# Optimization experiments

Hardware: AMD Instinct MI355X
Metric: run time of the kernel (lower is better)

Reference implementation:

```python
import jax, jax.numpy as jnp
import numpy as np

N = 10000
E = 320000
NDIM_IN = 128
EDIM = 128
NDIM_OUT = 128
HID = 152  # size_embedding
NCLS = 15  # nbclasses


def _lin(k, out_f, in_f, scale=0.05):
    kw, kb = jax.random.split(k)
    W = jax.random.normal(kw, (out_f, in_f), dtype=jnp.float32) * scale
    b = jax.random.normal(kb, (out_f,), dtype=jnp.float32) * scale
    return W, b


def setup_inputs() -> dict:
    key = jax.random.key(0)
    ks = jax.random.split(key, 12)
    nfeats = jax.random.normal(ks[0], (N, 1, NDIM_IN), dtype=jnp.float32)
    efeats = jax.random.normal(ks[1], (E, 1, EDIM), dtype=jnp.float32)
    src = jax.random.randint(ks[2], (E,), 0, N)
    dst = jax.random.randint(ks[3], (E,), 0, N)
    # SAGE layer 1: msg (ndim_in+edim -> 152), apply (ndim_in+152 -> 152)
    Wm1, bm1 = _lin(ks[4], HID, NDIM_IN + EDIM)
    Wa1, ba1 = _lin(ks[5], HID, NDIM_IN + HID)
    # layer 2: msg (152+edim -> 152), apply (152+152 -> 152)
    Wm2, bm2 = _lin(ks[6], HID, HID + EDIM)
    Wa2, ba2 = _lin(ks[7], HID, HID + HID)
    # layer 3: msg (152+edim -> ndim_out), apply (152+ndim_out -> ndim_out)
    Wm3, bm3 = _lin(ks[8], NDIM_OUT, HID + EDIM)
    Wa3, ba3 = _lin(ks[9], NDIM_OUT, HID + NDIM_OUT)
    # edge predictor: Linear(2*ndim_out -> nbclasses)
    Wp, bp = _lin(ks[10], NCLS, 2 * NDIM_OUT)
    return {"nfeats": nfeats, "efeats": efeats, "src": src, "dst": dst,
            "Wm1": Wm1, "bm1": bm1, "Wa1": Wa1, "ba1": ba1,
            "Wm2": Wm2, "bm2": bm2, "Wa2": Wa2, "ba2": ba2,
            "Wm3": Wm3, "bm3": bm3, "Wa3": Wa3, "ba3": ba3,
            "Wp": Wp, "bp": bp}


def _sage_layer(h, e, src, dst, Wm, bm, Wa, ba):
    # h: [N,1,din]  e: [E,1,edim]
    msg = jnp.concatenate([h[src], e], axis=-1) @ Wm.T + bm  # [E,1,dout]
    agg = jax.ops.segment_sum(msg, dst, num_segments=N)       # [N,1,dout]
    deg = jax.ops.segment_sum(jnp.ones((E,), dtype=h.dtype), dst, num_segments=N)
    h_neigh = agg / jnp.maximum(deg, 1.0)[:, None, None]      # mean; 0 for isolated nodes
    return jax.nn.relu(jnp.concatenate([h, h_neigh], axis=-1) @ Wa.T + ba)


def reference(nfeats, efeats, src, dst,
              Wm1, bm1, Wa1, ba1, Wm2, bm2, Wa2, ba2,
              Wm3, bm3, Wa3, ba3, Wp, bp):
    h = _sage_layer(nfeats, efeats, src, dst, Wm1, bm1, Wa1, ba1)
    h = _sage_layer(h, efeats, src, dst, Wm2, bm2, Wa2, ba2)  # dropout is identity in eval
    h = _sage_layer(h, efeats, src, dst, Wm3, bm3, Wa3, ba3)
    h = h.sum(axis=1)  # [N, ndim_out]
    v = jnp.concatenate([h[src], h[dst]], axis=1)  # [E, 2*ndim_out]
    return v @ Wp.T + bp  # [E, nbclasses]
```

## Files before the change

kernel.cpp:

```cpp
#include <hip/hip_runtime.h>
#include <hip/hip_bf16.h>
#include <cstdint>


static inline int cdiv(int a, int b) { return (a + b - 1) / b; }

#define NN 10000
#define NE 320000
#define MTB 313
#define MD 192

typedef __attribute__((ext_vector_type(8))) short bf16x8;
typedef __attribute__((ext_vector_type(4))) float f32x4;

__device__ __forceinline__ ushort f2bf(float x) {
  union { float f; unsigned u; } c; c.f = x;
  unsigned r = c.u + 0x7FFFu + ((c.u >> 16) & 1u);
  return (ushort)(r >> 16);
}
__device__ __forceinline__ float bf2f(unsigned h) {
  union { unsigned u; float f; } c; c.u = h << 16;
  return c.f;
}
__device__ __forceinline__ f32x4 mfma3(bf16x8 ah, bf16x8 al, bf16x8 bh, bf16x8 bl,
                                       f32x4 acc) {
  acc = __builtin_amdgcn_mfma_f32_16x16x32_bf16(ah, bh, acc, 0, 0, 0);
  acc = __builtin_amdgcn_mfma_f32_16x16x32_bf16(al, bh, acc, 0, 0, 0);
  acc = __builtin_amdgcn_mfma_f32_16x16x32_bf16(ah, bl, acc, 0, 0, 0);
  return acc;
}
__device__ __forceinline__ void ld32frag(const float* p, bf16x8& h, bf16x8& l) {
  float4 x0 = *(const float4*)p;
  float4 x1 = *(const float4*)(p + 4);
  float v[8] = {x0.x, x0.y, x0.z, x0.w, x1.x, x1.y, x1.z, x1.w};
#pragma unroll
  for (int j = 0; j < 8; ++j) {
    ushort hh = f2bf(v[j]);
    h[j] = (short)hh;
    l[j] = (short)f2bf(v[j] - bf2f(hh));
  }
}
__device__ __forceinline__ void wpack4(ushort* lds, int base, int KT, int row,
                                       int k0, float4 v) {
  int idx0 = base + ((k0 >> 5) * 4 + ((k0 >> 3) & 3)) * 256 + row * 8 + (k0 & 7);
  int idx1 = idx0 + KT * 1024;
  ushort h0 = f2bf(v.x), h1 = f2bf(v.y), h2 = f2bf(v.z), h3 = f2bf(v.w);
  uint2 uh, ul;
  uh.x = (unsigned)h0 | ((unsigned)h1 << 16);
  uh.y = (unsigned)h2 | ((unsigned)h3 << 16);
  ushort l0 = f2bf(v.x - bf2f(h0)), l1 = f2bf(v.y - bf2f(h1));
  ushort l2 = f2bf(v.z - bf2f(h2)), l3 = f2bf(v.w - bf2f(h3));
  ul.x = (unsigned)l0 | ((unsigned)l1 << 16);
  ul.y = (unsigned)l2 | ((unsigned)l3 << 16);
  *reinterpret_cast<uint2*>(&lds[idx0]) = uh;
  *reinterpret_cast<uint2*>(&lds[idx1]) = ul;
}
__device__ __forceinline__ bf16x8 rfrag(const ushort* lds, int base, int KT,
                                        int plane, int kt, int lane, int mh) {
  int idx = base + ((plane * KT + kt) * 4 + (lane >> 4)) * 256 +
            ((lane & 15) + 16 * mh) * 8;
  return *reinterpret_cast<const bf16x8*>(&lds[idx]);
}

__global__ __launch_bounds__(256) void k_bucket(const int* __restrict__ src,
                                                const int* __restrict__ dst,
                                                int* __restrict__ fill,
                                                int2* __restrict__ bk) {
  int e = blockIdx.x * 256 + threadIdx.x;
  if (e < NE) {
    int d = dst[e];
    int pos = atomicAdd(&fill[d], 1);
    if (pos < MD) bk[d * MD + pos] = make_int2(e, src[e]);
  }
}

struct WDesc {
  const float* W; ushort* hi; ushort* lo;
  int dout, KA, KApad, KB, Korig, NG16, KT, pred;
};
struct PrepArgs {
  WDesc d[7];
  int* fill;
};

__global__ __launch_bounds__(256) void k_prep(PrepArgs P) {
  const int y = blockIdx.y;
  if (y == 7) {
    int i = blockIdx.x * 256 + threadIdx.x;
    if (i < NN) P.fill[i] = 0;
    return;
  }
  const WDesc d = P.d[y];
  int tid = blockIdx.x * 256 + threadIdx.x;
  if (tid >= d.KT * d.NG16 * 64) return;
  int lane = tid & 63;
  int g = (tid >> 6) % d.NG16;
  int t = (tid >> 6) / d.NG16;
  int col = g * 16 + (lane & 15);
  int kbase = t * 32 + ((lane >> 4) * 8);
  size_t o = (size_t)tid * 8;
#pragma unroll
  for (int j = 0; j < 8; ++j) {
    int kk = kbase + j;
    float w = 0.f;
    if (!d.pred) {
      if (col < d.dout) {
        if (kk < d.KApad) { if (kk < d.KA) w = d.W[(size_t)col * d.Korig + kk]; }
        else { int kb = kk - d.KApad; if (kb < d.KB) w = d.W[(size_t)col * d.Korig + d.KA + kb]; }
      }
    } else {
      if (col < 15) w = d.W[(size_t)col * 256 + kk];
      else if (col < 30) w = d.W[(size_t)(col - 15) * 256 + 128 + kk];
    }
    ushort h = f2bf(w);
    d.hi[o + j] = h;
    d.lo[o + j] = f2bf(w - bf2f(h));
  }
}

__global__ __launch_bounds__(1024) void k_eaggpe(
    const float* __restrict__ efeats, const int2* __restrict__ bk,
    const int* __restrict__ fill, const float* __restrict__ nfeats,
    const ushort* __restrict__ Wm1h, const ushort* __restrict__ Wm1l,
    const ushort* __restrict__ pW1h, const ushort* __restrict__ pW1l,
    const ushort* __restrict__ pW2h, const ushort* __restrict__ pW2l,
    const ushort* __restrict__ pW3h, const ushort* __restrict__ pW3l,
    const float* __restrict__ bm1, const float* __restrict__ bm2,
    const float* __restrict__ bm3, float* __restrict__ deg_g,
    ushort* __restrict__ ph1, float* __restrict__ pe1,
    float* __restrict__ pe2, float* __restrict__ pe3) {
  __shared__ ushort efrag[2 * 4 * 1024];
  __shared__ float sdeg[32];
  const int tid = threadIdx.x;
  const int wid = tid >> 6, lane = tid & 63;
  const int row0 = blockIdx.x * 32;
  const int half = lane >> 5, cl = lane & 31;
#pragma unroll
  for (int i = 0; i < 2; ++i) {
    const int r = wid * 2 + i;
    const int d = row0 + r;
    float4 acc[8];
#pragma unroll
    for (int u = 0; u < 8; ++u) acc[u] = make_float4(0.f, 0.f, 0.f, 0.f);
    int cntd = 0;
    if (d < NN) {
      cntd = fill[d];
      const int n = min(cntd, MD);
      const int s = d * MD, t = s + n;
      int j = s;
      for (; j + 15 < t; j += 16) {
#pragma unroll
        for (int u = 0; u < 8; ++u) {
          int e0 = bk[j + 2 * u + half].x;
          float4 v = *(const float4*)(efeats + (size_t)e0 * 128 + cl * 4);
          acc[u].x += v.x; acc[u].y += v.y; acc[u].z += v.z; acc[u].w += v.w;
        }
      }
      for (; j + 1 < t; j += 2) {
        int e0 = bk[j + half].x;
        float4 v = *(const float4*)(efeats + (size_t)e0 * 128 + cl * 4);
        acc[0].x += v.x; acc[0].y += v.y; acc[0].z += v.z; acc[0].w += v.w;
      }
      if (j < t && half == 0) {
        int e0 = bk[j].x;
        float4 v = *(const float4*)(efeats + (size_t)e0 * 128 + cl * 4);
        acc[0].x += v.x; acc[0].y += v.y; acc[0].z += v.z; acc[0].w += v.w;
      }
    }
#pragma unroll
    for (int u = 4; u > 0; u >>= 1)
#pragma unroll
      for (int w = 0; w < u; ++w) {
        acc[w].x += acc[w + u].x; acc[w].y += acc[w + u].y;
        acc[w].z += acc[w + u].z; acc[w].w += acc[w + u].w;
      }
    float4 sm = acc[0];
    sm.x += __shfl_xor(sm.x, 32);
    sm.y += __shfl_xor(sm.y, 32);
    sm.z += __shfl_xor(sm.z, 32);
    sm.w += __shfl_xor(sm.w, 32);
    if (lane < 32) wpack4(efrag, 0, 4, r, cl * 4, sm);
    if (lane == 0) {
      sdeg[r] = (float)cntd;
      if (d < NN) deg_g[d] = (float)cntd;
    }
  }
  __syncthreads();
  const int rA = lane & 15, kl = (lane >> 4) * 8, colL = lane & 15;
  const int r0 = min(row0 + rA, NN - 1), r1 = min(row0 + 16 + rA, NN - 1);
  for (int j = wid; j < 19; j += 16) {
    const ushort *Wh, *Wl;
    const float* bm = nullptr;
    float* pe = nullptr;
    int NG16 = 10, ng0, WPAD = 160, dout = 152;
    bool proj = false;
    if (j < 5) { proj = true; Wh = Wm1h; Wl = Wm1l; ng0 = j * 2; }
    else if (j < 10) { Wh = pW1h; Wl = pW1l; bm = bm1; pe = pe1; ng0 = (j - 5) * 2; }
    else if (j < 15) { Wh = pW2h; Wl = pW2l; bm = bm2; pe = pe2; ng0 = (j - 10) * 2; }
    else { Wh = pW3h; Wl = pW3l; bm = bm3; pe = pe3; ng0 = (j - 15) * 2;
           NG16 = 8; WPAD = 128; dout = 128; }
    f32x4 a00 = {0.f, 0.f, 0.f, 0.f}, a01 = {0.f, 0.f, 0.f, 0.f};
    f32x4 a10 = {0.f, 0.f, 0.f, 0.f}, a11 = {0.f, 0.f, 0.f, 0.f};
#pragma unroll
    for (int kt = 0; kt < 4; ++kt) {
      bf16x8 a0h, a0l, a1h, a1l;
      if (proj) {
        ld32frag(nfeats + (size_t)r0 * 128 + kt * 32 + kl, a0h, a0l);
        ld32frag(nfeats + (size_t)r1 * 128 + kt * 32 + kl, a1h, a1l);
      } else {
        a0h = rfrag(efrag, 0, 4, 0, kt, lane, 0);
        a0l = rfrag(efrag, 0, 4, 1, kt, lane, 0);
        a1h = rfrag(efrag, 0, 4, 0, kt, lane, 1);
        a1l = rfrag(efrag, 0, 4, 1, kt, lane, 1);
      }
      size_t wb = ((size_t)(kt * NG16 + ng0) * 64 + lane) * 8;
      bf16x8 b0h = *(const bf16x8*)(Wh + wb), b0l = *(const bf16x8*)(Wl + wb);
      bf16x8 b1h = *(const bf16x8*)(Wh + wb + 512), b1l = *(const bf16x8*)(Wl + wb + 512);
      a00 = mfma3(a0h, a0l, b0h, b0l, a00);
      a01 = mfma3(a0h, a0l, b1h, b1l, a01);
      a10 = mfma3(a1h, a1l, b0h, b0l, a10);
      a11 = mfma3(a1h, a1l, b1h, b1l, a11);
    }
#pragma unroll
    for (int ms = 0; ms < 2; ++ms) {
      const f32x4 aN0 = ms ? a10 : a00;
      const f32x4 aN1 = ms ? a11 : a01;
#pragma unroll
      for (int reg = 0; reg < 4; ++reg) {
        int rloc = ms * 16 + (lane >> 4) * 4 + reg;
        int row = row0 + rloc;
        if (row >= NN) continue;
#pragma unroll
        for (int ns = 0; ns < 2; ++ns) {
          int col = (ng0 + ns) * 16 + colL;
          float v = ns ? aN1[reg] : aN0[reg];
          if (proj) {
            ph1[(size_t)row * 160 + col] = f2bf(col < 152 ? v : 0.f);
          } else {
            pe[(size_t)row * WPAD + col] =
                (col < dout) ? v + sdeg[rloc] * bm[col] : 0.f;
          }
        }
      }
    }
  }
}

template <int WP>
__global__ __launch_bounds__(64) void k_gath(const ushort* __restrict__ ph,
                                             const float* __restrict__ pe,
                                             const float* __restrict__ deg,
                                             const int2* __restrict__ bk,
                                             const int* __restrict__ fill,
                                             ushort* __restrict__ nmh,
                                             ushort* __restrict__ nml) {
  constexpr int PAIRS = WP / 2;
  constexpr int NV = (PAIRS + 63) / 64;
  const int d = blockIdx.x, lane = threadIdx.x;
  const int n = min(fill[d], MD);
  const int s = d * MD, t = s + n;
  float2 acc[NV][4];
#pragma unroll
  for (int v = 0; v < NV; ++v)
#pragma unroll
    for (int u = 0; u < 4; ++u) acc[v][u] = make_float2(0.f, 0.f);
  int j = s;
  for (; j + 3 < t; j += 4) {
    int s0 = bk[j].y, s1 = bk[j + 1].y, s2 = bk[j + 2].y, s3 = bk[j + 3].y;
#pragma unroll
    for (int v = 0; v < NV; ++v) {
      int p = lane + 64 * v;
      if (p < PAIRS) {
        unsigned x0 = *(const unsigned*)(ph + (size_t)s0 * WP + 2 * p);
        unsigned x1 = *(const unsigned*)(ph + (size_t)s1 * WP + 2 * p);
        unsigned x2 = *(const unsigned*)(ph + (size_t)s2 * WP + 2 * p);
        unsigned x3 = *(const unsigned*)(ph + (size_t)s3 * WP + 2 * p);
        acc[v][0].x += bf2f(x0 & 0xffffu); acc[v][0].y += bf2f(x0 >> 16);
        acc[v][1].x += bf2f(x1 & 0xffffu); acc[v][1].y += bf2f(x1 >> 16);
        acc[v][2].x += bf2f(x2 & 0xffffu); acc[v][2].y += bf2f(x2 >> 16);
        acc[v][3].x += bf2f(x3 & 0xffffu); acc[v][3].y += bf2f(x3 >> 16);
      }
    }
  }
  for (; j < t; ++j) {
    int s0 = bk[j].y;
#pragma unroll
    for (int v = 0; v < NV; ++v) {
      int p = lane + 64 * v;
      if (p < PAIRS) {
        unsigned x0 = *(const unsigned*)(ph + (size_t)s0 * WP + 2 * p);
        acc[v][0].x += bf2f(x0 & 0xffffu); acc[v][0].y += bf2f(x0 >> 16);
      }
    }
  }
  const float inv = 1.f / fmaxf(deg[d], 1.f);
#pragma unroll
  for (int v = 0; v < NV; ++v) {
    int p = lane + 64 * v;
    if (p < PAIRS) {
      float sx = (acc[v][0].x + acc[v][1].x) + (acc[v][2].x + acc[v][3].x);
      float sy = (acc[v][0].y + acc[v][1].y) + (acc[v][2].y + acc[v][3].y);
      float2 pv = *(const float2*)(pe + (size_t)d * WP + 2 * p);
      float nx = (sx + pv.x) * inv, ny = (sy + pv.y) * inv;
      size_t o = (size_t)d * WP + 2 * p;
      ushort hx = f2bf(nx), hy = f2bf(ny);
      *(unsigned*)(nmh + o) = (unsigned)hx | ((unsigned)hy << 16);
      *(unsigned*)(nml + o) =
          (unsigned)f2bf(nx - bf2f(hx)) | ((unsigned)f2bf(ny - bf2f(hy)) << 16);
    }
  }
}

template <int KTH, int KTNM, int NGA, int NGP, bool PRED, bool A32>
__global__ __launch_bounds__(NGA * 32) void k_applyproj(
    const ushort* __restrict__ Ahi, const ushort* __restrict__ Alo,
    const float* __restrict__ Af,
    const ushort* __restrict__ nmh, const ushort* __restrict__ nml,
    const ushort* __restrict__ Wah, const ushort* __restrict__ Wal,
    const float* __restrict__ ba,
    ushort* __restrict__ Yhi, ushort* __restrict__ Ylo,
    const ushort* __restrict__ Wnh, const ushort* __restrict__ Wnl,
    ushort* __restrict__ phout, float* __restrict__ hsd,
    int dout_a, int dout_p) {
  constexpr int KTO = NGA / 2;
  constexpr int OSTR = KTO * 32;
  constexpr int SA = KTH * 32, SB = KTNM * 32;
  constexpr int OSTR2 = NGP * 16;
  __shared__ ushort lds[2 * KTO * 1024];
  const int tid = threadIdx.x;
  const int wid = tid >> 6, lane = tid & 63;
  const int rA = lane & 15, kl = (lane >> 4) * 8, colL = lane & 15;
  const int q = lane >> 4;
  const int row0 = blockIdx.x * 32;
  const int r0 = min(row0 + rA, NN - 1), r1 = min(row0 + 16 + rA, NN - 1);
  {
    const int ng0 = wid * 2;
    f32x4 a00 = {0.f, 0.f, 0.f, 0.f}, a01 = {0.f, 0.f, 0.f, 0.f};
    f32x4 a10 = {0.f, 0.f, 0.f, 0.f}, a11 = {0.f, 0.f, 0.f, 0.f};
#pragma unroll
    for (int kt = 0; kt < KTH + KTNM; ++kt) {
      bf16x8 a0h, a0l, a1h, a1l;
      if (kt < KTH) {
        if constexpr (A32) {
          ld32frag(Af + (size_t)r0 * SA + kt * 32 + kl, a0h, a0l);
          ld32frag(Af + (size_t)r1 * SA + kt * 32 + kl, a1h, a1l);
        } else {
          size_t o0 = (size_t)r0 * SA + kt * 32 + kl;
          size_t o1 = (size_t)r1 * SA + kt * 32 + kl;
          a0h = *(const bf16x8*)(Ahi + o0); a0l = *(const bf16x8*)(Alo + o0);
          a1h = *(const bf16x8*)(Ahi + o1); a1l = *(const bf16x8*)(Alo + o1);
        }
      } else {
        int kb = (kt - KTH) * 32 + kl;
        size_t o0 = (size_t)r0 * SB + kb, o1 = (size_t)r1 * SB + kb;
        a0h = *(const bf16x8*)(nmh + o0); a0l = *(const bf16x8*)(nml + o0);
        a1h = *(const bf16x8*)(nmh + o1); a1l = *(const bf16x8*)(nml + o1);
      }
      size_t wb = ((size_t)(kt * NGA + ng0) * 64 + lane) * 8;
      bf16x8 b0h = *(const bf16x8*)(Wah + wb), b0l = *(const bf16x8*)(Wal + wb);
      bf16x8 b1h = *(const bf16x8*)(Wah + wb + 512), b1l = *(const bf16x8*)(Wal + wb + 512);
      a00 = mfma3(a0h, a0l, b0h, b0l, a00);
      a01 = mfma3(a0h, a0l, b1h, b1l, a01);
      a10 = mfma3(a1h, a1l, b0h, b0l, a10);
      a11 = mfma3(a1h, a1l, b1h, b1l, a11);
    }
#pragma unroll
    for (int ms = 0; ms < 2; ++ms) {
      const f32x4 aN0 = ms ? a10 : a00;
      const f32x4 aN1 = ms ? a11 : a01;
#pragma unroll
      for (int reg = 0; reg < 4; ++reg) {
        int rloc = ms * 16 + (lane >> 4) * 4 + reg;
        int row = row0 + rloc;
#pragma unroll
        for (int ns = 0; ns < 2; ++ns) {
          int col = (ng0 + ns) * 16 + colL;
          float v = ns ? aN1[reg] : aN0[reg];
          float y = (col < dout_a) ? fmaxf(v + ba[col], 0.f) : 0.f;
          ushort h = f2bf(y), l = f2bf(y - bf2f(h));
          int idx = ((col >> 5) * 4 + ((col >> 3) & 3)) * 256 + rloc * 8 + (col & 7);
          lds[idx] = h;
          lds[idx + KTO * 1024] = l;
          if constexpr (!PRED) {
            if (row < NN) {
              Yhi[(size_t)row * OSTR + col] = h;
              Ylo[(size_t)row * OSTR + col] = l;
            }
          }
        }
      }
    }
  }
  __syncthreads();
  if (wid < NGP / 2) {
    const int ng0 = wid * 2;
    f32x4 a00 = {0.f, 0.f, 0.f, 0.f}, a01 = {0.f, 0.f, 0.f, 0.f};
    f32x4 a10 = {0.f, 0.f, 0.f, 0.f}, a11 = {0.f, 0.f, 0.f, 0.f};
#pragma unroll
    for (int kt = 0; kt < KTO; ++kt) {
      int b0 = (kt * 4 + q) * 256;
      int b1 = ((KTO + kt) * 4 + q) * 256;
      bf16x8 a0h = *(const bf16x8*)(lds + b0 + rA * 8);
      bf16x8 a1h = *(const bf16x8*)(lds + b0 + (rA + 16) * 8);
      bf16x8 a0l = *(const bf16x8*)(lds + b1 + rA * 8);
      bf16x8 a1l = *(const bf16x8*)(lds + b1 + (rA + 16) * 8);
      size_t wb = ((size_t)(kt * NGP + ng0) * 64 + lane) * 8;
      bf16x8 b0h = *(const bf16x8*)(Wnh + wb), b0l = *(const bf16x8*)(Wnl + wb);
      bf16x8 b1h = *(const bf16x8*)(Wnh + wb + 512), b1l = *(const bf16x8*)(Wnl + wb + 512);
      a00 = mfma3(a0h, a0l, b0h, b0l, a00);
      a01 = mfma3(a0h, a0l, b1h, b1l, a01);
      a10 = mfma3(a1h, a1l, b0h, b0l, a10);
      a11 = mfma3(a1h, a1l, b1h, b1l, a11);
    }
#pragma unroll
    for (int ms = 0; ms < 2; ++ms) {
      const f32x4 aN0 = ms ? a10 : a00;
      const f32x4 aN1 = ms ? a11 : a01;
#pragma unroll
      for (int reg = 0; reg < 4; ++reg) {
        int row = row0 + ms * 16 + (lane >> 4) * 4 + reg;
        if (row >= NN) continue;
#pragma unroll
        for (int ns = 0; ns < 2; ++ns) {
          int col = (ng0 + ns) * 16 + colL;
          float v = ns ? aN1[reg] : aN0[reg];
          if constexpr (PRED)
            hsd[(size_t)row * 32 + col] = v;
          else
            phout[(size_t)row * OSTR2 + col] = f2bf(col < dout_p ? v : 0.f);
        }
      }
    }
  }
}

__global__ __launch_bounds__(256) void k_edge_out(const int* __restrict__ src,
                                                  const int* __restrict__ dst,
                                                  const float* __restrict__ hsd,
                                                  const float* __restrict__ bp,
                                                  float* __restrict__ out) {
  int i = blockIdx.x * 256 + threadIdx.x;
  if (i >= NE * 15) return;
  int e = i / 15, c = i - e * 15;
  out[i] = hsd[(size_t)src[e] * 32 + c] + hsd[(size_t)dst[e] * 32 + 15 + c] + bp[c];
}

extern "C" void kernel_launch(void* const* d_in, const int* in_sizes, int n_in,
                              void* d_out, int out_size, void* d_ws, size_t ws_size,
                              hipStream_t stream) {
  const float* nfeats = (const float*)d_in[0];
  const float* efeats = (const float*)d_in[1];
  const int* src = (const int*)d_in[2];
  const int* dst = (const int*)d_in[3];
  const float* Wm1 = (const float*)d_in[4];
  const float* bm1 = (const float*)d_in[5];
  const float* Wa1 = (const float*)d_in[6];
  const float* ba1 = (const float*)d_in[7];
  const float* Wm2 = (const float*)d_in[8];
  const float* bm2 = (const float*)d_in[9];
  const float* Wa2 = (const float*)d_in[10];
  const float* ba2 = (const float*)d_in[11];
  const float* Wm3 = (const float*)d_in[12];
  const float* bm3 = (const float*)d_in[13];
  const float* Wa3 = (const float*)d_in[14];
  const float* ba3 = (const float*)d_in[15];
  const float* Wp = (const float*)d_in[16];
  const float* bp = (const float*)d_in[17];
  float* out = (float*)d_out;

  char* base = (char*)d_ws;
  size_t woff = 0;
  auto alloc = [&](size_t bytes) -> void* {
    void* p = base + woff;
    woff += (bytes + 255) & ~(size_t)255;
    return p;
  };
  int* fill = (int*)alloc((size_t)NN * 4);
  int2* bk = (int2*)alloc((size_t)NN * MD * 8);
  float* deg = (float*)alloc((size_t)NN * 4);
  auto aplane = [&](int w) { return (ushort*)alloc((size_t)NN * w * 2); };
  ushort* h1h = aplane(160); ushort* h1l = aplane(160);
  ushort* h2h = aplane(160); ushort* h2l = aplane(160);
  ushort* nmh = aplane(160); ushort* nml = aplane(160);
  ushort* ph1 = aplane(160); ushort* ph2 = aplane(160);
  float* pe1 = (float*)alloc((size_t)NN * 160 * 4);
  float* pe2 = (float*)alloc((size_t)NN * 160 * 4);
  float* pe3 = (float*)alloc((size_t)NN * 128 * 4);
  float* hsd = (float*)alloc((size_t)NN * 32 * 4);
  auto wpk = [&](int kt, int ng) { return (ushort*)alloc((size_t)kt * ng * 512 * 2); };
  ushort* Wm1h = wpk(8, 10);  ushort* Wm1l = wpk(8, 10);
  ushort* Wa1h = wpk(9, 10);  ushort* Wa1l = wpk(9, 10);
  ushort* Wm2h = wpk(9, 10);  ushort* Wm2l = wpk(9, 10);
  ushort* Wa2h = wpk(10, 10); ushort* Wa2l = wpk(10, 10);
  ushort* Wm3h = wpk(9, 8);   ushort* Wm3l = wpk(9, 8);
  ushort* Wa3h = wpk(9, 8);   ushort* Wa3l = wpk(9, 8);
  ushort* Wpph = wpk(4, 2);   ushort* Wppl = wpk(4, 2);

  PrepArgs pa;
  pa.d[0] = {Wm1, Wm1h, Wm1l, 152, 128, 128, 128, 256, 10, 8, 0};
  pa.d[1] = {Wa1, Wa1h, Wa1l, 152, 128, 128, 152, 280, 10, 9, 0};
  pa.d[2] = {Wm2, Wm2h, Wm2l, 152, 152, 160, 128, 280, 10, 9, 0};
  pa.d[3] = {Wa2, Wa2h, Wa2l, 152, 152, 160, 152, 304, 10, 10, 0};
  pa.d[4] = {Wm3, Wm3h, Wm3l, 128, 152, 160, 128, 280, 8, 9, 0};
  pa.d[5] = {Wa3, Wa3h, Wa3l, 128, 152, 160, 128, 280, 8, 9, 0};
  pa.d[6] = {Wp, Wpph, Wppl, 32, 128, 128, 0, 256, 2, 4, 1};
  pa.fill = fill;
  k_prep<<<dim3(40, 8), 256, 0, stream>>>(pa);

  k_bucket<<<cdiv(NE, 256), 256, 0, stream>>>(src, dst, fill, bk);

  k_eaggpe<<<MTB, 1024, 0, stream>>>(
      efeats, bk, fill, nfeats, Wm1h, Wm1l,
      Wm1h + (size_t)4 * 10 * 512, Wm1l + (size_t)4 * 10 * 512,
      Wm2h + (size_t)5 * 10 * 512, Wm2l + (size_t)5 * 10 * 512,
      Wm3h + (size_t)5 * 8 * 512, Wm3l + (size_t)5 * 8 * 512,
      bm1, bm2, bm3, deg, ph1, pe1, pe2, pe3);

  k_gath<160><<<NN, 64, 0, stream>>>(ph1, pe1, deg, bk, fill, nmh, nml);
  k_applyproj<4, 5, 10, 10, false, true><<<MTB, 320, 0, stream>>>(
      nullptr, nullptr, nfeats, nmh, nml, Wa1h, Wa1l, ba1,
      h1h, h1l, Wm2h, Wm2l, ph2, nullptr, 152, 152);
  k_gath<160><<<NN, 64, 0, stream>>>(ph2, pe2, deg, bk, fill, nmh, nml);
  k_applyproj<5, 5, 10, 8, false, false><<<MTB, 320, 0, stream>>>(
      h1h, h1l, nullptr, nmh, nml, Wa2h, Wa2l, ba2,
      h2h, h2l, Wm3h, Wm3l, ph1, nullptr, 152, 128);
  k_gath<128><<<NN, 64, 0, stream>>>(ph1, pe3, deg, bk, fill, nmh, nml);
  k_applyproj<5, 4, 8, 2, true, false><<<MTB, 256, 0, stream>>>(
      h2h, h2l, nullptr, nmh, nml, Wa3h, Wa3l, ba3,
      nullptr, nullptr, Wpph, Wppl, nullptr, hsd, 128, 32);

  k_edge_out<<<cdiv(NE * 15, 256), 256, 0, stream>>>(src, dst, hsd, bp, out);
}
```

Before: 225.6 us.

## Move edge-aggregate projections into apply kernels and split aggregation into per-node blocks

The fused 1024-thread aggregation kernel becomes per-node 64-thread blocks that store the summed edge features as bf16 hi/lo planes, plus extra blocks that do the layer-1 message projection. Each layer's edge-sum projection through Wm's edge half, the bias times degree, and the mean division now happen inside the apply kernel, written to LDS and consumed directly. The gather kernels emit raw fp32 sums instead of normalized hi/lo planes. This removes the pe1/pe2/pe3 buffers and the nm round-trip through global memory, at the cost of redoing the edge projection work in each apply kernel and using more LDS there.

```diff
diff --git a/kernel.cpp b/kernel.cpp
--- a/kernel.cpp
+++ b/kernel.cpp
@@ -40,20 +40,12 @@
     l[j] = (short)f2bf(v[j] - bf2f(hh));
   }
 }
-__device__ __forceinline__ void wpack4(ushort* lds, int base, int KT, int row,
-                                       int k0, float4 v) {
-  int idx0 = base + ((k0 >> 5) * 4 + ((k0 >> 3) & 3)) * 256 + row * 8 + (k0 & 7);
-  int idx1 = idx0 + KT * 1024;
-  ushort h0 = f2bf(v.x), h1 = f2bf(v.y), h2 = f2bf(v.z), h3 = f2bf(v.w);
-  uint2 uh, ul;
-  uh.x = (unsigned)h0 | ((unsigned)h1 << 16);
-  uh.y = (unsigned)h2 | ((unsigned)h3 << 16);
-  ushort l0 = f2bf(v.x - bf2f(h0)), l1 = f2bf(v.y - bf2f(h1));
-  ushort l2 = f2bf(v.z - bf2f(h2)), l3 = f2bf(v.w - bf2f(h3));
-  ul.x = (unsigned)l0 | ((unsigned)l1 << 16);
-  ul.y = (unsigned)l2 | ((unsigned)l3 << 16);
-  *reinterpret_cast<uint2*>(&lds[idx0]) = uh;
-  *reinterpret_cast<uint2*>(&lds[idx1]) = ul;
+__device__ __forceinline__ void wpack1(ushort* lds, int base, int KT, int row,
+                                       int k, float v) {
+  int idx0 = base + ((k >> 5) * 4 + ((k >> 3) & 3)) * 256 + row * 8 + (k & 7);
+  ushort h = f2bf(v);
+  lds[idx0] = h;
+  lds[idx0 + KT * 1024] = f2bf(v - bf2f(h));
 }
 __device__ __forceinline__ bf16x8 rfrag(const ushort* lds, int base, int KT,
                                         int plane, int kt, int lane, int mh) {
@@ -118,54 +110,40 @@
   }
 }
 
-__global__ __launch_bounds__(1024) void k_eaggpe(
+__global__ __launch_bounds__(64) void k_eaggproj(
     const float* __restrict__ efeats, const int2* __restrict__ bk,
     const int* __restrict__ fill, const float* __restrict__ nfeats,
     const ushort* __restrict__ Wm1h, const ushort* __restrict__ Wm1l,
-    const ushort* __restrict__ pW1h, const ushort* __restrict__ pW1l,
-    const ushort* __restrict__ pW2h, const ushort* __restrict__ pW2l,
-    const ushort* __restrict__ pW3h, const ushort* __restrict__ pW3l,
-    const float* __restrict__ bm1, const float* __restrict__ bm2,
-    const float* __restrict__ bm3, float* __restrict__ deg_g,
-    ushort* __restrict__ ph1, float* __restrict__ pe1,
-    float* __restrict__ pe2, float* __restrict__ pe3) {
-  __shared__ ushort efrag[2 * 4 * 1024];
-  __shared__ float sdeg[32];
-  const int tid = threadIdx.x;
-  const int wid = tid >> 6, lane = tid & 63;
-  const int row0 = blockIdx.x * 32;
-  const int half = lane >> 5, cl = lane & 31;
-#pragma unroll
-  for (int i = 0; i < 2; ++i) {
-    const int r = wid * 2 + i;
-    const int d = row0 + r;
+    ushort* __restrict__ ehi, ushort* __restrict__ elo,
+    float* __restrict__ deg, ushort* __restrict__ ph1) {
+  const int lane = threadIdx.x;
+  if (blockIdx.x < NN) {
+    const int d = blockIdx.x;
+    const int half = lane >> 5, cl = lane & 31;
+    const int cntd = fill[d];
+    const int n = min(cntd, MD);
+    const int s = d * MD, t = s + n;
     float4 acc[8];
 #pragma unroll
     for (int u = 0; u < 8; ++u) acc[u] = make_float4(0.f, 0.f, 0.f, 0.f);
-    int cntd = 0;
-    if (d < NN) {
-      cntd = fill[d];
-      const int n = min(cntd, MD);
-      const int s = d * MD, t = s + n;
-      int j = s;
-      for (; j + 15 < t; j += 16) {
-#pragma unroll
-        for (int u = 0; u < 8; ++u) {
-          int e0 = bk[j + 2 * u + half].x;
-          float4 v = *(const float4*)(efeats + (size_t)e0 * 128 + cl * 4);
-          acc[u].x += v.x; acc[u].y += v.y; acc[u].z += v.z; acc[u].w += v.w;
-        }
-      }
-      for (; j + 1 < t; j += 2) {
-        int e0 = bk[j + half].x;
+    int j = s;
+    for (; j + 15 < t; j += 16) {
+#pragma unroll
+      for (int u = 0; u < 8; ++u) {
+        int e0 = bk[j + 2 * u + half].x;
         float4 v = *(const float4*)(efeats + (size_t)e0 * 128 + cl * 4);
-        acc[0].x += v.x; acc[0].y += v.y; acc[0].z += v.z; acc[0].w += v.w;
-      }
-      if (j < t && half == 0) {
-        int e0 = bk[j].x;
-        float4 v = *(const float4*)(efeats + (size_t)e0 * 128 + cl * 4);
-        acc[0].x += v.x; acc[0].y += v.y; acc[0].z += v.z; acc[0].w += v.w;
-      }
+        acc[u].x += v.x; acc[u].y += v.y; acc[u].z += v.z; acc[u].w += v.w;
+      }
+    }
+    for (; j + 1 < t; j += 2) {
+      int e0 = bk[j + half].x;
+      float4 v = *(const float4*)(efeats + (size_t)e0 * 128 + cl * 4);
+      acc[0].x += v.x; acc[0].y += v.y; acc[0].z += v.z; acc[0].w += v.w;
+    }
+    if (j < t && half == 0) {
+      int e0 = bk[j].x;
+      float4 v = *(const float4*)(efeats + (size_t)e0 * 128 + cl * 4);
+      acc[0].x += v.x; acc[0].y += v.y; acc[0].z += v.z; acc[0].w += v.w;
     }
 #pragma unroll
     for (int u = 4; u > 0; u >>= 1)
@@ -179,68 +157,53 @@
     sm.y += __shfl_xor(sm.y, 32);
     sm.z += __shfl_xor(sm.z, 32);
     sm.w += __shfl_xor(sm.w, 32);
-    if (lane < 32) wpack4(efrag, 0, 4, r, cl * 4, sm);
-    if (lane == 0) {
-      sdeg[r] = (float)cntd;
-      if (d < NN) deg_g[d] = (float)cntd;
-    }
-  }
-  __syncthreads();
+    if (lane < 32) {
+      size_t o = (size_t)d * 128 + cl * 4;
+      ushort h0 = f2bf(sm.x), h1 = f2bf(sm.y), h2 = f2bf(sm.z), h3 = f2bf(sm.w);
+      uint2 uh, ul;
+      uh.x = (unsigned)h0 | ((unsigned)h1 << 16);
+      uh.y = (unsigned)h2 | ((unsigned)h3 << 16);
+      ul.x = (unsigned)f2bf(sm.x - bf2f(h0)) | ((unsigned)f2bf(sm.y - bf2f(h1)) << 16);
+      ul.y = (unsigned)f2bf(sm.z - bf2f(h2)) | ((unsigned)f2bf(sm.w - bf2f(h3)) << 16);
+      *(uint2*)(ehi + o) = uh;
+      *(uint2*)(elo + o) = ul;
+    }
+    if (lane == 0) deg[d] = (float)cntd;
+    return;
+  }
+  const int p = blockIdx.x - NN;
+  const int ng0 = (p % 5) * 2;
+  const int row0 = (p / 5) * 32;
   const int rA = lane & 15, kl = (lane >> 4) * 8, colL = lane & 15;
   const int r0 = min(row0 + rA, NN - 1), r1 = min(row0 + 16 + rA, NN - 1);
-  for (int j = wid; j < 19; j += 16) {
-    const ushort *Wh, *Wl;
-    const float* bm = nullptr;
-    float* pe = nullptr;
-    int NG16 = 10, ng0, WPAD = 160, dout = 152;
-    bool proj = false;
-    if (j < 5) { proj = true; Wh = Wm1h; Wl = Wm1l; ng0 = j * 2; }
-    else if (j < 10) { Wh = pW1h; Wl = pW1l; bm = bm1; pe = pe1; ng0 = (j - 5) * 2; }
-    else if (j < 15) { Wh = pW2h; Wl = pW2l; bm = bm2; pe = pe2; ng0 = (j - 10) * 2; }
-    else { Wh = pW3h; Wl = pW3l; bm = bm3; pe = pe3; ng0 = (j - 15) * 2;
-           NG16 = 8; WPAD = 128; dout = 128; }
-    f32x4 a00 = {0.f, 0.f, 0.f, 0.f}, a01 = {0.f, 0.f, 0.f, 0.f};
-    f32x4 a10 = {0.f, 0.f, 0.f, 0.f}, a11 = {0.f, 0.f, 0.f, 0.f};
-#pragma unroll
-    for (int kt = 0; kt < 4; ++kt) {
-      bf16x8 a0h, a0l, a1h, a1l;
-      if (proj) {
-        ld32frag(nfeats + (size_t)r0 * 128 + kt * 32 + kl, a0h, a0l);
-        ld32frag(nfeats + (size_t)r1 * 128 + kt * 32 + kl, a1h, a1l);
-      } else {
-        a0h = rfrag(efrag, 0, 4, 0, kt, lane, 0);
-        a0l = rfrag(efrag, 0, 4, 1, kt, lane, 0);
-        a1h = rfrag(efrag, 0, 4, 0, kt, lane, 1);
-        a1l = rfrag(efrag, 0, 4, 1, kt, lane, 1);
-      }
-      size_t wb = ((size_t)(kt * NG16 + ng0) * 64 + lane) * 8;
-      bf16x8 b0h = *(const bf16x8*)(Wh + wb), b0l = *(const bf16x8*)(Wl + wb);
-      bf16x8 b1h = *(const bf16x8*)(Wh + wb + 512), b1l = *(const bf16x8*)(Wl + wb + 512);
-      a00 = mfma3(a0h, a0l, b0h, b0l, a00);
-      a01 = mfma3(a0h, a0l, b1h, b1l, a01);
-      a10 = mfma3(a1h, a1l, b0h, b0l, a10);
-      a11 = mfma3(a1h, a1l, b1h, b1l, a11);
-    }
-#pragma unroll
-    for (int ms = 0; ms < 2; ++ms) {
-      const f32x4 aN0 = ms ? a10 : a00;
-      const f32x4 aN1 = ms ? a11 : a01;
-#pragma unroll
-      for (int reg = 0; reg < 4; ++reg) {
-        int rloc = ms * 16 + (lane >> 4) * 4 + reg;
-        int row = row0 + rloc;
-        if (row >= NN) continue;
-#pragma unroll
-        for (int ns = 0; ns < 2; ++ns) {
-          int col = (ng0 + ns) * 16 + colL;
-          float v = ns ? aN1[reg] : aN0[reg];
-          if (proj) {
-            ph1[(size_t)row * 160 + col] = f2bf(col < 152 ? v : 0.f);
-          } else {
-            pe[(size_t)row * WPAD + col] =
-                (col < dout) ? v + sdeg[rloc] * bm[col] : 0.f;
-          }
-        }
+  f32x4 a00 = {0.f, 0.f, 0.f, 0.f}, a01 = {0.f, 0.f, 0.f, 0.f};
+  f32x4 a10 = {0.f, 0.f, 0.f, 0.f}, a11 = {0.f, 0.f, 0.f, 0.f};
+#pragma unroll
+  for (int kt = 0; kt < 4; ++kt) {
+    bf16x8 a0h, a0l, a1h, a1l;
+    ld32frag(nfeats + (size_t)r0 * 128 + kt * 32 + kl, a0h, a0l);
+    ld32frag(nfeats + (size_t)r1 * 128 + kt * 32 + kl, a1h, a1l);
+    size_t wb = ((size_t)(kt * 10 + ng0) * 64 + lane) * 8;
+    bf16x8 b0h = *(const bf16x8*)(Wm1h + wb), b0l = *(const bf16x8*)(Wm1l + wb);
+    bf16x8 b1h = *(const bf16x8*)(Wm1h + wb + 512), b1l = *(const bf16x8*)(Wm1l + wb + 512);
+    a00 = mfma3(a0h, a0l, b0h, b0l, a00);
+    a01 = mfma3(a0h, a0l, b1h, b1l, a01);
+    a10 = mfma3(a1h, a1l, b0h, b0l, a10);
+    a11 = mfma3(a1h, a1l, b1h, b1l, a11);
+  }
+#pragma unroll
+  for (int ms = 0; ms < 2; ++ms) {
+    const f32x4 aN0 = ms ? a10 : a00;
+    const f32x4 aN1 = ms ? a11 : a01;
+#pragma unroll
+    for (int reg = 0; reg < 4; ++reg) {
+      int row = row0 + ms * 16 + (lane >> 4) * 4 + reg;
+      if (row >= NN) continue;
+#pragma unroll
+      for (int ns = 0; ns < 2; ++ns) {
+        int col = (ng0 + ns) * 16 + colL;
+        float v = ns ? aN1[reg] : aN0[reg];
+        ph1[(size_t)row * 160 + col] = f2bf(col < 152 ? v : 0.f);
       }
     }
   }
@@ -248,74 +211,58 @@
 
 template <int WP>
 __global__ __launch_bounds__(64) void k_gath(const ushort* __restrict__ ph,
-                                             const float* __restrict__ pe,
-                                             const float* __restrict__ deg,
                                              const int2* __restrict__ bk,
                                              const int* __restrict__ fill,
-                                             ushort* __restrict__ nmh,
-                                             ushort* __restrict__ nml) {
-  constexpr int PAIRS = WP / 2;
-  constexpr int NV = (PAIRS + 63) / 64;
+                                             float* __restrict__ gsum) {
+  constexpr int QUADS = WP / 4;
   const int d = blockIdx.x, lane = threadIdx.x;
   const int n = min(fill[d], MD);
   const int s = d * MD, t = s + n;
-  float2 acc[NV][4];
-#pragma unroll
-  for (int v = 0; v < NV; ++v)
-#pragma unroll
-    for (int u = 0; u < 4; ++u) acc[v][u] = make_float2(0.f, 0.f);
+  float4 a0 = {0.f, 0.f, 0.f, 0.f}, a1 = a0, a2 = a0, a3 = a0;
   int j = s;
   for (; j + 3 < t; j += 4) {
     int s0 = bk[j].y, s1 = bk[j + 1].y, s2 = bk[j + 2].y, s3 = bk[j + 3].y;
-#pragma unroll
-    for (int v = 0; v < NV; ++v) {
-      int p = lane + 64 * v;
-      if (p < PAIRS) {
-        unsigned x0 = *(const unsigned*)(ph + (size_t)s0 * WP + 2 * p);
-        unsigned x1 = *(const unsigned*)(ph + (size_t)s1 * WP + 2 * p);
-        unsigned x2 = *(const unsigned*)(ph + (size_t)s2 * WP + 2 * p);
-        unsigned x3 = *(const unsigned*)(ph + (size_t)s3 * WP + 2 * p);
-        acc[v][0].x += bf2f(x0 & 0xffffu); acc[v][0].y += bf2f(x0 >> 16);
-        acc[v][1].x += bf2f(x1 & 0xffffu); acc[v][1].y += bf2f(x1 >> 16);
-        acc[v][2].x += bf2f(x2 & 0xffffu); acc[v][2].y += bf2f(x2 >> 16);
-        acc[v][3].x += bf2f(x3 & 0xffffu); acc[v][3].y += bf2f(x3 >> 16);
-      }
+    if (lane < QUADS) {
+      uint2 u0 = *(const uint2*)(ph + (size_t)s0 * WP + 4 * lane);
+      uint2 u1 = *(const uint2*)(ph + (size_t)s1 * WP + 4 * lane);
+      uint2 u2 = *(const uint2*)(ph + (size_t)s2 * WP + 4 * lane);
+      uint2 u3 = *(const uint2*)(ph + (size_t)s3 * WP + 4 * lane);
+      a0.x += bf2f(u0.x & 0xffffu); a0.y += bf2f(u0.x >> 16);
+      a0.z += bf2f(u0.y & 0xffffu); a0.w += bf2f(u0.y >> 16);
+      a1.x += bf2f(u1.x & 0xffffu); a1.y += bf2f(u1.x >> 16);
+      a1.z += bf2f(u1.y & 0xffffu); a1.w += bf2f(u1.y >> 16);
+      a2.x += bf2f(u2.x & 0xffffu); a2.y += bf2f(u2.x >> 16);
+      a2.z += bf2f(u2.y & 0xffffu); a2.w += bf2f(u2.y >> 16);
+      a3.x += bf2f(u3.x & 0xffffu); a3.y += bf2f(u3.x >> 16);
+      a3.z += bf2f(u3.y & 0xffffu); a3.w += bf2f(u3.y >> 16);
     }
   }
   for (; j < t; ++j) {
     int s0 = bk[j].y;
-#pragma unroll
-    for (int v = 0; v < NV; ++v) {
-      int p = lane + 64 * v;
-      if (p < PAIRS) {
-        unsigned x0 = *(const unsigned*)(ph + (size_t)s0 * WP + 2 * p);
-        acc[v][0].x += bf2f(x0 & 0xffffu); acc[v][0].y += bf2f(x0 >> 16);
-      }
-    }
-  }
-  const float inv = 1.f / fmaxf(deg[d], 1.f);
-#pragma unroll
-  for (int v = 0; v < NV; ++v) {
-    int p = lane + 64 * v;
-    if (p < PAIRS) {
-      float sx = (acc[v][0].x + acc[v][1].x) + (acc[v][2].x + acc[v][3].x);
-      float sy = (acc[v][0].y + acc[v][1].y) + (acc[v][2].y + acc[v][3].y);
-      float2 pv = *(const float2*)(pe + (size_t)d * WP + 2 * p);
-      float nx = (sx + pv.x) * inv, ny = (sy + pv.y) * inv;
-      size_t o = (size_t)d * WP + 2 * p;
-      ushort hx = f2bf(nx), hy = f2bf(ny);
-      *(unsigned*)(nmh + o) = (unsigned)hx | ((unsigned)hy << 16);
-      *(unsigned*)(nml + o) =
-          (unsigned)f2bf(nx - bf2f(hx)) | ((unsigned)f2bf(ny - bf2f(hy)) << 16);
-    }
+    if (lane < QUADS) {
+      uint2 u0 = *(const uint2*)(ph + (size_t)s0 * WP + 4 * lane);
+      a0.x += bf2f(u0.x & 0xffffu); a0.y += bf2f(u0.x >> 16);
+      a0.z += bf2f(u0.y & 0xffffu); a0.w += bf2f(u0.y >> 16);
+    }
+  }
+  if (lane < QUADS) {
+    float4 r;
+    r.x = (a0.x + a1.x) + (a2.x + a3.x);
+    r.y = (a0.y + a1.y) + (a2.y + a3.y);
+    r.z = (a0.z + a1.z) + (a2.z + a3.z);
+    r.w = (a0.w + a1.w) + (a2.w + a3.w);
+    *(float4*)(gsum + (size_t)d * WP + 4 * lane) = r;
   }
 }
 
 template <int KTH, int KTNM, int NGA, int NGP, bool PRED, bool A32>
 __global__ __launch_bounds__(NGA * 32) void k_applyproj(
     const ushort* __restrict__ Ahi, const ushort* __restrict__ Alo,
-    const float* __restrict__ Af,
-    const ushort* __restrict__ nmh, const ushort* __restrict__ nml,
+    const float* __restrict__ Af, const float* __restrict__ gsum,
+    const ushort* __restrict__ eah, const ushort* __restrict__ eal,
+    const ushort* __restrict__ Wmeh, const ushort* __restrict__ Wmel,
+    const float* __restrict__ bm, const float* __restrict__ deg,
+    int NG16M, int dout_m,
     const ushort* __restrict__ Wah, const ushort* __restrict__ Wal,
     const float* __restrict__ ba,
     ushort* __restrict__ Yhi, ushort* __restrict__ Ylo,
@@ -324,16 +271,59 @@
     int dout_a, int dout_p) {
   constexpr int KTO = NGA / 2;
   constexpr int OSTR = KTO * 32;
-  constexpr int SA = KTH * 32, SB = KTNM * 32;
+  constexpr int SA = KTH * 32;
+  constexpr int WPAD = KTNM * 32;
   constexpr int OSTR2 = NGP * 16;
-  __shared__ ushort lds[2 * KTO * 1024];
+  constexpr int BASE_OUT = 2 * KTNM * 1024;
+  __shared__ ushort lds[BASE_OUT + 2 * KTO * 1024];
   const int tid = threadIdx.x;
   const int wid = tid >> 6, lane = tid & 63;
   const int rA = lane & 15, kl = (lane >> 4) * 8, colL = lane & 15;
   const int q = lane >> 4;
   const int row0 = blockIdx.x * 32;
   const int r0 = min(row0 + rA, NN - 1), r1 = min(row0 + 16 + rA, NN - 1);
-  {
+  if (wid < KTNM) {
+    const int ng0 = wid * 2;
+    f32x4 a00 = {0.f, 0.f, 0.f, 0.f}, a01 = {0.f, 0.f, 0.f, 0.f};
+    f32x4 a10 = {0.f, 0.f, 0.f, 0.f}, a11 = {0.f, 0.f, 0.f, 0.f};
+#pragma unroll
+    for (int kt = 0; kt < 4; ++kt) {
+      size_t o0 = (size_t)r0 * 128 + kt * 32 + kl;
+      size_t o1 = (size_t)r1 * 128 + kt * 32 + kl;
+      bf16x8 a0h = *(const bf16x8*)(eah + o0), a0l = *(const bf16x8*)(eal + o0);
+      bf16x8 a1h = *(const bf16x8*)(eah + o1), a1l = *(const bf16x8*)(eal + o1);
+      size_t wb = ((size_t)(kt * NG16M + ng0) * 64 + lane) * 8;
+      bf16x8 b0h = *(const bf16x8*)(Wmeh + wb), b0l = *(const bf16x8*)(Wmel + wb);
+      bf16x8 b1h = *(const bf16x8*)(Wmeh + wb + 512), b1l = *(const bf16x8*)(Wmel + wb + 512);
+      a00 = mfma3(a0h, a0l, b0h, b0l, a00);
+      a01 = mfma3(a0h, a0l, b1h, b1l, a01);
+      a10 = mfma3(a1h, a1l, b0h, b0l, a10);
+      a11 = mfma3(a1h, a1l, b1h, b1l, a11);
+    }
+#pragma unroll
+    for (int ms = 0; ms < 2; ++ms) {
+      const f32x4 aN0 = ms ? a10 : a00;
+      const f32x4 aN1 = ms ? a11 : a01;
+#pragma unroll
+      for (int reg = 0; reg < 4; ++reg) {
+        int rloc = ms * 16 + (lane >> 4) * 4 + reg;
+        int row = row0 + rloc;
+        float dg = (row < NN) ? deg[row] : 0.f;
+        float inv = 1.f / fmaxf(dg, 1.f);
+#pragma unroll
+        for (int ns = 0; ns < 2; ++ns) {
+          int col = (ng0 + ns) * 16 + colL;
+          float acc = ns ? aN1[reg] : aN0[reg];
+          float y = 0.f;
+          if (col < dout_m && row < NN)
+            y = (gsum[(size_t)row * WPAD + col] + acc + dg * bm[col]) * inv;
+          wpack1(lds, 0, KTNM, rloc, col, y);
+        }
+      }
+    }
+  }
+  __syncthreads();
+  if (wid < NGA / 2) {
     const int ng0 = wid * 2;
     f32x4 a00 = {0.f, 0.f, 0.f, 0.f}, a01 = {0.f, 0.f, 0.f, 0.f};
     f32x4 a10 = {0.f, 0.f, 0.f, 0.f}, a11 = {0.f, 0.f, 0.f, 0.f};
@@ -351,10 +341,11 @@
           a1h = *(const bf16x8*)(Ahi + o1); a1l = *(const bf16x8*)(Alo + o1);
         }
       } else {
-        int kb = (kt - KTH) * 32 + kl;
-        size_t o0 = (size_t)r0 * SB + kb, o1 = (size_t)r1 * SB + kb;
-        a0h = *(const bf16x8*)(nmh + o0); a0l = *(const bf16x8*)(nml + o0);
-        a1h = *(const bf16x8*)(nmh + o1); a1l = *(const bf16x8*)(nml + o1);
+        const int rkt = kt - KTH;
+        a0h = rfrag(lds, 0, KTNM, 0, rkt, lane, 0);
+        a0l = rfrag(lds, 0, KTNM, 1, rkt, lane, 0);
+        a1h = rfrag(lds, 0, KTNM, 0, rkt, lane, 1);
+        a1l = rfrag(lds, 0, KTNM, 1, rkt, lane, 1);
       }
       size_t wb = ((size_t)(kt * NGA + ng0) * 64 + lane) * 8;
       bf16x8 b0h = *(const bf16x8*)(Wah + wb), b0l = *(const bf16x8*)(Wal + wb);
@@ -378,7 +369,7 @@
           float v = ns ? aN1[reg] : aN0[reg];
           float y = (col < dout_a) ? fmaxf(v + ba[col], 0.f) : 0.f;
           ushort h = f2bf(y), l = f2bf(y - bf2f(h));
-          int idx = ((col >> 5) * 4 + ((col >> 3) & 3)) * 256 + rloc * 8 + (col & 7);
+          int idx = BASE_OUT + ((col >> 5) * 4 + ((col >> 3) & 3)) * 256 + rloc * 8 + (col & 7);
           lds[idx] = h;
           lds[idx + KTO * 1024] = l;
           if constexpr (!PRED) {
@@ -398,8 +389,8 @@
     f32x4 a10 = {0.f, 0.f, 0.f, 0.f}, a11 = {0.f, 0.f, 0.f, 0.f};
 #pragma unroll
     for (int kt = 0; kt < KTO; ++kt) {
-      int b0 = (kt * 4 + q) * 256;
-      int b1 = ((KTO + kt) * 4 + q) * 256;
+      int b0 = BASE_OUT + (kt * 4 + q) * 256;
+      int b1 = BASE_OUT + ((KTO + kt) * 4 + q) * 256;
       bf16x8 a0h = *(const bf16x8*)(lds + b0 + rA * 8);
       bf16x8 a1h = *(const bf16x8*)(lds + b0 + (rA + 16) * 8);
       bf16x8 a0l = *(const bf16x8*)(lds + b1 + rA * 8);
@@ -479,13 +470,11 @@
   int2* bk = (int2*)alloc((size_t)NN * MD * 8);
   float* deg = (float*)alloc((size_t)NN * 4);
   auto aplane = [&](int w) { return (ushort*)alloc((size_t)NN * w * 2); };
+  ushort* eah = aplane(128); ushort* eal = aplane(128);
   ushort* h1h = aplane(160); ushort* h1l = aplane(160);
   ushort* h2h = aplane(160); ushort* h2l = aplane(160);
-  ushort* nmh = aplane(160); ushort* nml = aplane(160);
   ushort* ph1 = aplane(160); ushort* ph2 = aplane(160);
-  float* pe1 = (float*)alloc((size_t)NN * 160 * 4);
-  float* pe2 = (float*)alloc((size_t)NN * 160 * 4);
-  float* pe3 = (float*)alloc((size_t)NN * 128 * 4);
+  float* gsum = (float*)alloc((size_t)NN * 160 * 4);
   float* hsd = (float*)alloc((size_t)NN * 32 * 4);
   auto wpk = [&](int kt, int ng) { return (ushort*)alloc((size_t)kt * ng * 512 * 2); };
   ushort* Wm1h = wpk(8, 10);  ushort* Wm1l = wpk(8, 10);
@@ -509,25 +498,24 @@
 
   k_bucket<<<cdiv(NE, 256), 256, 0, stream>>>(src, dst, fill, bk);
 
-  k_eaggpe<<<MTB, 1024, 0, stream>>>(
-      efeats, bk, fill, nfeats, Wm1h, Wm1l,
-      Wm1h + (size_t)4 * 10 * 512, Wm1l + (size_t)4 * 10 * 512,
-      Wm2h + (size_t)5 * 10 * 512, Wm2l + (size_t)5 * 10 * 512,
-      Wm3h + (size_t)5 * 8 * 512, Wm3l + (size_t)5 * 8 * 512,
-      bm1, bm2, bm3, deg, ph1, pe1, pe2, pe3);
-
-  k_gath<160><<<NN, 64, 0, stream>>>(ph1, pe1, deg, bk, fill, nmh, nml);
+  k_eaggproj<<<NN + 5 * MTB, 64, 0, stream>>>(
+      efeats, bk, fill, nfeats, Wm1h, Wm1l, eah, eal, deg, ph1);
+
+  k_gath<160><<<NN, 64, 0, stream>>>(ph1, bk, fill, gsum);
   k_applyproj<4, 5, 10, 10, false, true><<<MTB, 320, 0, stream>>>(
-      nullptr, nullptr, nfeats, nmh, nml, Wa1h, Wa1l, ba1,
-      h1h, h1l, Wm2h, Wm2l, ph2, nullptr, 152, 152);
-  k_gath<160><<<NN, 64, 0, stream>>>(ph2, pe2, deg, bk, fill, nmh, nml);
+      nullptr, nullptr, nfeats, gsum, eah, eal,
+      Wm1h + (size_t)4 * 10 * 512, Wm1l + (size_t)4 * 10 * 512, bm1, deg, 10, 152,
+      Wa1h, Wa1l, ba1, h1h, h1l, Wm2h, Wm2l, ph2, nullptr, 152, 152);
+  k_gath<160><<<NN, 64, 0, stream>>>(ph2, bk, fill, gsum);
   k_applyproj<5, 5, 10, 8, false, false><<<MTB, 320, 0, stream>>>(
-      h1h, h1l, nullptr, nmh, nml, Wa2h, Wa2l, ba2,
-      h2h, h2l, Wm3h, Wm3l, ph1, nullptr, 152, 128);
-  k_gath<128><<<NN, 64, 0, stream>>>(ph1, pe3, deg, bk, fill, nmh, nml);
+      h1h, h1l, nullptr, gsum, eah, eal,
+      Wm2h + (size_t)5 * 10 * 512, Wm2l + (size_t)5 * 10 * 512, bm2, deg, 10, 152,
+      Wa2h, Wa2l, ba2, h2h, h2l, Wm3h, Wm3l, ph1, nullptr, 152, 128);
+  k_gath<128><<<NN, 64, 0, stream>>>(ph1, bk, fill, gsum);
   k_applyproj<5, 4, 8, 2, true, false><<<MTB, 256, 0, stream>>>(
-      h2h, h2l, nullptr, nmh, nml, Wa3h, Wa3l, ba3,
-      nullptr, nullptr, Wpph, Wppl, nullptr, hsd, 128, 32);
+      h2h, h2l, nullptr, gsum, eah, eal,
+      Wm3h + (size_t)5 * 8 * 512, Wm3l + (size_t)5 * 8 * 512, bm3, deg, 8, 128,
+      Wa3h, Wa3l, ba3, nullptr, nullptr, Wpph, Wppl, nullptr, hsd, 128, 32);
 
   k_edge_out<<<cdiv(NE * 15, 256), 256, 0, stream>>>(src, dst, hsd, bp, out);
 }
```

Result: faster. 219.4 us (-2.7%).
